# Optimization experiments

Hardware: AMD Instinct MI355X
Metric: run time of the kernel (lower is better)

## Reference

```python
import jax, jax.numpy as jnp
import numpy as np

PAIRS = [(0,1),(1,2),(2,3),(0,4),(4,5),(5,6),(0,7),(7,8),(8,9),(9,10),(8,11),(11,12),(12,13),(8,14),(14,15),(15,16)]
END_JOINTS = np.array([3, 6, 10, 13, 16])  # leaf joints gated in the trailing loop
N, DIM, HID, B = 17, 512, 384, 8192
LN_EPS = 1e-5


def _build_adj():
    A = np.zeros((N, N), np.float32)
    for p, c in PAIRS:
        A[p, c] = A[c, p] = 1.0
    A += np.eye(N, dtype=np.float32)
    dinv = 1.0 / np.sqrt(A.sum(1))
    return jnp.asarray(dinv[:, None] * A * dinv[None, :])


def setup_inputs() -> dict:
    key = jax.random.key(0)
    ks = jax.random.split(key, 8)
    return {
        "x_gcn": jax.random.normal(ks[0], (B, N, DIM), jnp.float32),
        "bone_features": jax.random.normal(ks[1], (B, N, 192), jnp.float32),
        "adj": _build_adj(),
        "g1": jnp.ones((DIM,), jnp.float32),
        "b1": jnp.zeros((DIM,), jnp.float32),
        "W1": jax.random.normal(ks[2], (2, DIM, HID), jnp.float32) * 0.02,
        "M1": jax.random.uniform(ks[3], (N, HID), jnp.float32),
        "A2_1": jnp.ones((N, N), jnp.float32),
        "bias1": jnp.zeros((HID,), jnp.float32),
        "W2": jax.random.normal(ks[4], (2, HID, DIM), jnp.float32) * 0.02,
        "M2": jax.random.uniform(ks[5], (N, DIM), jnp.float32),
        "A2_2": jnp.ones((N, N), jnp.float32),
        "bias2": jnp.zeros((DIM,), jnp.float32),
        "g2": jnp.ones((DIM,), jnp.float32),
        "b2": jnp.zeros((DIM,), jnp.float32),
    }


def _ln(x, g, b):
    m = x.mean(-1, keepdims=True)
    v = jnp.mean((x - m) ** 2, axis=-1, keepdims=True)
    return (x - m) * jax.lax.rsqrt(v + LN_EPS) * g + b


def _mgc(x, W, M, adj_base, A2, bias):
    # Modulated graph conv: separate self / neighbor transforms, per-node modulation M.
    h0 = jnp.einsum('bnc,cd->bnd', x, W[0])
    h1 = jnp.einsum('bnc,cd->bnd', x, W[1])
    adj = adj_base + A2
    adj = (adj.T + adj) * 0.5
    E = jnp.eye(N, dtype=x.dtype)
    out = jnp.einsum('vw,bwd->bvd', adj * E, M * h0) + jnp.einsum('vw,bwd->bvd', adj * (1.0 - E), M * h1)
    return out + bias


def reference(x_gcn, bone_features, adj, g1, b1, W1, M1, A2_1, bias1,
              W2, M2, A2_2, bias2, g2, b2):
    h = _ln(x_gcn, g1, b1)
    h = _mgc(h, W1, M1, adj, A2_1, bias1)
    h = jax.nn.gelu(h, approximate=False)  # torch nn.GELU default = exact erf
    h = _mgc(h, W2, M2, adj, A2_2, bias2)
    h = _ln(h, g2, b2)
    xp = x_gcn + h  # drop_path=0 -> identity

    # bone gating: first chunk(3, -1) slice, mean over channels, sigmoid gate
    c = bone_features.shape[-1]
    bone_chunk = bone_features[..., : -(-c // 3)]  # torch.chunk first piece (ceil)
    gate = jax.nn.sigmoid(bone_chunk.mean(-1, keepdims=True) * 0.01)  # (B, N, 1)
    mask = jnp.zeros((N,), xp.dtype).at[jnp.asarray(END_JOINTS)].set(1.0)
    return xp * (1.0 + 0.03 * gate * mask[None, :, None])
```

## Files before the change

### kernel.cpp

```cpp
#include <hip/hip_runtime.h>
#include <hip/hip_bf16.h>

typedef __attribute__((ext_vector_type(8))) short s16x8;
typedef __attribute__((ext_vector_type(4))) float f32x4;

typedef __attribute__((address_space(1))) void v_as1;
typedef __attribute__((address_space(3))) void v_as3;

__device__ __forceinline__ void gload16(const void* g, void* l) {
    __builtin_amdgcn_global_load_lds((const v_as1*)g, (v_as3*)l, 16, 0, 0);
}

__device__ __forceinline__ unsigned short f2bf(float f) {
    unsigned u = __float_as_uint(f);
    unsigned r = (u + 0x7FFFu + ((u >> 16) & 1u)) >> 16;
    return (unsigned short)r;
}
__device__ __forceinline__ float frombf(unsigned short u) {
    return __uint_as_float(((unsigned)u) << 16);
}

__device__ __forceinline__ float gelu_fast(float v) {
    float ax = fabsf(v) * 0.70710678118f;
    float t = __builtin_amdgcn_rcpf(fmaf(0.3275911f, ax, 1.f));
    float poly = t * fmaf(t, fmaf(t, fmaf(t, fmaf(t, 1.061405429f, -1.453152027f),
                                          1.421413741f), -0.284496736f), 0.254829592f);
    float e = exp2f(ax * ax * -1.44269504089f);
    float er = fmaf(-poly, e, 1.f);
    er = copysignf(er, v);
    return 0.5f * v * (1.f + er);
}

__global__ void prep_w1(const float* __restrict__ W1, unsigned short* __restrict__ w1t) {
    int idx = blockIdx.x * 256 + threadIdx.x;
    if (idx >= 768 * 512) return;
    int n = idx >> 9, k = idx & 511;
    int g = (n >= 384) ? 1 : 0;
    int d = n - g * 384;
    w1t[idx] = f2bf(W1[((long)g * 512 + k) * 384 + d]);
}

__global__ void prep_w2(const float* __restrict__ W2, unsigned short* __restrict__ w2t) {
    int idx = blockIdx.x * 256 + threadIdx.x;
    if (idx >= 1024 * 384) return;
    int n = idx / 384, k = idx % 384;
    int g = (n >= 512) ? 1 : 0;
    int d = n - g * 512;
    w2t[idx] = f2bf(W2[((long)g * 384 + k) * 512 + d]);
}

__global__ void prep_adj(const float* __restrict__ adj, const float* __restrict__ A2a,
                         const float* __restrict__ A2b, float* __restrict__ coef1,
                         float* __restrict__ coef2) {
    int t = threadIdx.x;
    if (t < 289) {
        int v = t / 17, w = t % 17;
        int tt = w * 17 + v;
        float s1 = 0.5f * (adj[t] + A2a[t] + adj[tt] + A2a[tt]);
        float s2 = 0.5f * (adj[t] + A2b[t] + adj[tt] + A2b[tt]);
        coef1[t] = (v == w) ? 0.f : s1;
        coef2[t] = (v == w) ? 0.f : s2;
        if (v == w) { coef1[289 + v] = s1; coef2[289 + v] = s2; }
    }
}

__global__ __launch_bounds__(256) void ln1_kernel(const float* __restrict__ x,
                                                  const float* __restrict__ g,
                                                  const float* __restrict__ b,
                                                  unsigned short* __restrict__ y, int rows) {
    int wave = threadIdx.x >> 6, lane = threadIdx.x & 63;
    long row = (long)blockIdx.x * 4 + wave;
    if (row >= rows) return;
    const float4* xr = (const float4*)(x + row * 512);
    float4 v0 = xr[lane];
    float4 v1 = xr[lane + 64];
    float s = v0.x + v0.y + v0.z + v0.w + v1.x + v1.y + v1.z + v1.w;
    float q = v0.x * v0.x + v0.y * v0.y + v0.z * v0.z + v0.w * v0.w +
              v1.x * v1.x + v1.y * v1.y + v1.z * v1.z + v1.w * v1.w;
    #pragma unroll
    for (int off = 32; off; off >>= 1) { s += __shfl_xor(s, off); q += __shfl_xor(q, off); }
    float mean = s * (1.f / 512.f);
    float var  = q * (1.f / 512.f) - mean * mean;
    float rstd = rsqrtf(var + 1e-5f);
    const float4* gr = (const float4*)g;
    const float4* br = (const float4*)b;
    ushort4* yr = (ushort4*)(y + row * 512);
    #pragma unroll
    for (int i = 0; i < 2; ++i) {
        float4 vv = i ? v1 : v0;
        float4 gg = gr[lane + 64 * i];
        float4 bb = br[lane + 64 * i];
        ushort4 o;
        o.x = f2bf((vv.x - mean) * rstd * gg.x + bb.x);
        o.y = f2bf((vv.y - mean) * rstd * gg.y + bb.y);
        o.z = f2bf((vv.z - mean) * rstd * gg.z + bb.z);
        o.w = f2bf((vv.w - mean) * rstd * gg.w + bb.w);
        yr[lane + 64 * i] = o;
    }
}

__global__ __launch_bounds__(256) void gemm_bt_kernel(const unsigned short* __restrict__ A,
                                                      const unsigned short* __restrict__ Bt,
                                                      unsigned short* __restrict__ C,
                                                      int K, int Ncols, int NBX) {
    __shared__ __align__(16) unsigned short As[128 * 64];
    __shared__ __align__(16) unsigned short Bs[128 * 64];
    const int t = threadIdx.x;
    const int lane = t & 63;
    const int w = t >> 6;
    const int wr = w >> 1, wc = w & 1;

    const int nwg = gridDim.x;
    const int q = nwg >> 3, r = nwg & 7;
    const int xcd = blockIdx.x & 7, pos = blockIdx.x >> 3;
    const int wgid = (xcd < r ? xcd * (q + 1) : r * (q + 1) + (xcd - r) * q) + pos;
    const int bx = wgid % NBX;
    const int by = wgid / NBX;
    const long row0 = (long)by * 128;
    const long col0 = (long)bx * 128;

    const int lm = lane & 15;
    const int g4 = lane >> 4;
    const int swz0 = ((g4 ^ (lm & 7)) * 8);
    const int swz1 = (((g4 + 4) ^ (lm & 7)) * 8);

    f32x4 acc[4][4];
    #pragma unroll
    for (int m = 0; m < 4; ++m)
        #pragma unroll
        for (int n = 0; n < 4; ++n) acc[m][n] = (f32x4)0.f;

    const int srow = t >> 3;
    const int sslot = (t & 7) ^ (srow & 7);
    const unsigned short* aBase = A + (row0 + srow) * K + sslot * 8;
    const unsigned short* bBase = Bt + (col0 + srow) * K + sslot * 8;
    unsigned short* aDst = &As[w * 512];
    unsigned short* bDst = &Bs[w * 512];

    const int ktiles = K >> 6;
    for (int kt = 0; kt < ktiles; ++kt) {
        const long ko = (long)kt * 64;
        __syncthreads();
        #pragma unroll
        for (int rr = 0; rr < 4; ++rr) {
            gload16(aBase + (long)(rr * 32) * K + ko, aDst + rr * 2048);
            gload16(bBase + (long)(rr * 32) * K + ko, bDst + rr * 2048);
        }
        __syncthreads();
        #pragma unroll
        for (int kk = 0; kk < 2; ++kk) {
            const int so = kk ? swz1 : swz0;
            s16x8 af[4], bfv[4];
            #pragma unroll
            for (int m = 0; m < 4; ++m)
                af[m] = *(const s16x8*)&As[(wr * 64 + m * 16 + lm) * 64 + so];
            #pragma unroll
            for (int n = 0; n < 4; ++n)
                bfv[n] = *(const s16x8*)&Bs[(wc * 64 + n * 16 + lm) * 64 + so];
            #pragma unroll
            for (int m = 0; m < 4; ++m)
                #pragma unroll
                for (int n = 0; n < 4; ++n)
                    acc[m][n] = __builtin_amdgcn_mfma_f32_16x16x32_bf16(af[m], bfv[n], acc[m][n], 0, 0, 0);
        }
    }
    const int r4 = (lane >> 4) * 4;
    #pragma unroll
    for (int m = 0; m < 4; ++m) {
        #pragma unroll
        for (int j = 0; j < 4; ++j) {
            long grow = row0 + wr * 64 + m * 16 + r4 + j;
            unsigned short* crow = C + grow * Ncols + col0 + wc * 64 + lm;
            #pragma unroll
            for (int n = 0; n < 4; ++n) crow[n * 16] = f2bf(acc[m][n][j]);
        }
    }
}

__global__ __launch_bounds__(384) void mixgelu_kernel(const unsigned short* __restrict__ h,
                                                      const float* __restrict__ M1,
                                                      const float* __restrict__ coef,
                                                      const float* __restrict__ bias,
                                                      unsigned short* __restrict__ z) {
    const int t = threadIdx.x;
    const int half = t / 192;
    const int tt = t - half * 192;
    const int d0 = tt * 2;
    const long b = blockIdx.x * 2 + half;
    const unsigned short* hb = h + b * 17 * 768;

    float ax[17], ay[17];
    const float bx = bias[d0], by = bias[d0 + 1];
    #pragma unroll
    for (int v = 0; v < 17; ++v) {
        float dg = coef[289 + v];
        float2 m = *(const float2*)(M1 + v * 384 + d0);
        ushort2 hv = *(const ushort2*)(hb + v * 768 + d0);
        ax[v] = dg * m.x * frombf(hv.x) + bx;
        ay[v] = dg * m.y * frombf(hv.y) + by;
    }
    #pragma unroll
    for (int w = 0; w < 17; ++w) {
        float2 m = *(const float2*)(M1 + w * 384 + d0);
        ushort2 hw = *(const ushort2*)(hb + w * 768 + 384 + d0);
        float px = m.x * frombf(hw.x);
        float py = m.y * frombf(hw.y);
        #pragma unroll
        for (int v = 0; v < 17; ++v) {
            float c = coef[v * 17 + w];
            ax[v] += c * px;
            ay[v] += c * py;
        }
    }
    unsigned short* zb = z + b * 17 * 384 + d0;
    #pragma unroll
    for (int v = 0; v < 17; ++v) {
        float gx = gelu_fast(ax[v]);
        float gy = gelu_fast(ay[v]);
        ushort2 o; o.x = f2bf(gx); o.y = f2bf(gy);
        *(ushort2*)(zb + v * 384) = o;
    }
}

__global__ __launch_bounds__(256) void final_kernel(const unsigned short* __restrict__ h2,
                                                    const float* __restrict__ x,
                                                    const float* __restrict__ bone,
                                                    const float* __restrict__ M2,
                                                    const float* __restrict__ coef,
                                                    const float* __restrict__ bias2,
                                                    const float* __restrict__ g2,
                                                    const float* __restrict__ b2,
                                                    float* __restrict__ out) {
    __shared__ float gate[17];
    __shared__ float red[17][8];
    const int t = threadIdx.x, lane = t & 63, wave = t >> 6;
    const int d0 = t * 2;
    const long b = blockIdx.x;

    #pragma unroll
    for (int v0 = 0; v0 < 20; v0 += 4) {
        int v = v0 + wave;
        if (v < 17) {
            float s = bone[(b * 17 + v) * 192 + lane];
            #pragma unroll
            for (int off = 32; off; off >>= 1) s += __shfl_xor(s, off);
            if (lane == 0) gate[v] = 1.f / (1.f + expf(-s * (0.01f / 64.f)));
        }
    }

    const unsigned short* hb = h2 + b * 17 * 1024;
    float ax[17], ay[17];
    const float bx = bias2[d0], by = bias2[d0 + 1];
    #pragma unroll
    for (int v = 0; v < 17; ++v) {
        float dg = coef[289 + v];
        float2 m = *(const float2*)(M2 + v * 512 + d0);
        ushort2 hv = *(const ushort2*)(hb + v * 1024 + d0);
        ax[v] = dg * m.x * frombf(hv.x) + bx;
        ay[v] = dg * m.y * frombf(hv.y) + by;
    }
    #pragma unroll
    for (int w = 0; w < 17; ++w) {
        float2 m = *(const float2*)(M2 + w * 512 + d0);
        ushort2 hw = *(const ushort2*)(hb + w * 1024 + 512 + d0);
        float px = m.x * frombf(hw.x);
        float py = m.y * frombf(hw.y);
        #pragma unroll
        for (int v = 0; v < 17; ++v) {
            float c = coef[v * 17 + w];
            ax[v] += c * px;
            ay[v] += c * py;
        }
    }
    #pragma unroll
    for (int v = 0; v < 17; ++v) {
        float s = ax[v] + ay[v];
        float q = ax[v] * ax[v] + ay[v] * ay[v];
        #pragma unroll
        for (int off = 32; off; off >>= 1) { s += __shfl_xor(s, off); q += __shfl_xor(q, off); }
        if (lane == 0) { red[v][wave] = s; red[v][4 + wave] = q; }
    }
    __syncthreads();
    const float2 gg = *(const float2*)(g2 + d0);
    const float2 bb = *(const float2*)(b2 + d0);
    const float* xb = x + b * 17 * 512 + d0;
    float* ob = out + b * 17 * 512 + d0;
    #pragma unroll
    for (int v = 0; v < 17; ++v) {
        float s = red[v][0] + red[v][1] + red[v][2] + red[v][3];
        float q = red[v][4] + red[v][5] + red[v][6] + red[v][7];
        float mean = s * (1.f / 512.f);
        float rstd = rsqrtf(q * (1.f / 512.f) - mean * mean + 1e-5f);
        const bool endj = (v == 3 || v == 6 || v == 10 || v == 13 || v == 16);
        float scale = endj ? (1.f + 0.03f * gate[v]) : 1.f;
        float2 xv = *(const float2*)(xb + v * 512);
        float ox = (xv.x + (ax[v] - mean) * rstd * gg.x + bb.x) * scale;
        float oy = (xv.y + (ay[v] - mean) * rstd * gg.y + bb.y) * scale;
        *(float2*)(ob + v * 512) = make_float2(ox, oy);
    }
}

extern "C" void kernel_launch(void* const* d_in, const int* in_sizes, int n_in,
                              void* d_out, int out_size, void* d_ws, size_t ws_size,
                              hipStream_t stream) {
    const float* x     = (const float*)d_in[0];
    const float* bone  = (const float*)d_in[1];
    const float* adj   = (const float*)d_in[2];
    const float* g1    = (const float*)d_in[3];
    const float* b1    = (const float*)d_in[4];
    const float* W1    = (const float*)d_in[5];
    const float* M1    = (const float*)d_in[6];
    const float* A21   = (const float*)d_in[7];
    const float* bias1 = (const float*)d_in[8];
    const float* W2    = (const float*)d_in[9];
    const float* M2    = (const float*)d_in[10];
    const float* A22   = (const float*)d_in[11];
    const float* bias2 = (const float*)d_in[12];
    const float* g2    = (const float*)d_in[13];
    const float* b2    = (const float*)d_in[14];
    float* out = (float*)d_out;

    char* ws = (char*)d_ws;
    size_t off = 0;
    auto alloc = [&](size_t bytes) -> char* {
        char* p = ws + off;
        off = (off + bytes + 255) & ~(size_t)255;
        return p;
    };
    unsigned short* w1t = (unsigned short*)alloc(768 * 512 * 2);
    unsigned short* w2t = (unsigned short*)alloc(1024 * 384 * 2);
    float* coef1 = (float*)alloc(306 * 4);
    float* coef2 = (float*)alloc(306 * 4);
    size_t fixed = off;

    int nc = 32;
    const int cands[6] = {1, 2, 4, 8, 16, 32};
    for (int ci = 0; ci < 6; ++ci) {
        size_t Bc = 8192 / cands[ci];
        size_t need = fixed + Bc * 17 * (512 + 768 + 384 + 1024) * 2 + 4 * 256;
        if (need <= ws_size) { nc = cands[ci]; break; }
    }
    long Bc = 8192 / nc;
    unsigned short* y  = (unsigned short*)alloc(Bc * 17 * 512 * 2);
    unsigned short* h  = (unsigned short*)alloc(Bc * 17 * 768 * 2);
    unsigned short* z  = (unsigned short*)alloc(Bc * 17 * 384 * 2);
    unsigned short* h2 = (unsigned short*)alloc(Bc * 17 * 1024 * 2);

    prep_w1<<<(768 * 512 + 255) / 256, 256, 0, stream>>>(W1, w1t);
    prep_w2<<<(1024 * 384 + 255) / 256, 256, 0, stream>>>(W2, w2t);
    prep_adj<<<1, 320, 0, stream>>>(adj, A21, A22, coef1, coef2);

    int rows = (int)(Bc * 17);
    int nby = rows / 128;
    for (int c = 0; c < nc; ++c) {
        long rb = (long)c * rows;
        ln1_kernel<<<rows / 4, 256, 0, stream>>>(x + rb * 512, g1, b1, y, rows);
        gemm_bt_kernel<<<6 * nby, 256, 0, stream>>>(y, w1t, h, 512, 768, 6);
        mixgelu_kernel<<<Bc / 2, 384, 0, stream>>>(h, M1, coef1, bias1, z);
        gemm_bt_kernel<<<8 * nby, 256, 0, stream>>>(z, w2t, h2, 384, 1024, 8);
        final_kernel<<<Bc, 256, 0, stream>>>(h2, x + rb * 512, bone + rb * 192, M2, coef2,
                                             bias2, g2, b2, out + rb * 512);
    }
}
```

Before: 693.2 us.

## Double-buffer LDS tiles in GEMM to overlap global loads with MFMA

```diff
diff --git a/kernel.cpp b/kernel.cpp
--- a/kernel.cpp
+++ b/kernel.cpp
@@ -103,8 +103,8 @@
                                                       const unsigned short* __restrict__ Bt,
                                                       unsigned short* __restrict__ C,
                                                       int K, int Ncols, int NBX) {
-    __shared__ __align__(16) unsigned short As[128 * 64];
-    __shared__ __align__(16) unsigned short Bs[128 * 64];
+    __shared__ __align__(16) unsigned short As[2][128 * 64];
+    __shared__ __align__(16) unsigned short Bs[2][128 * 64];
     const int t = threadIdx.x;
     const int lane = t & 63;
     const int w = t >> 6;
@@ -134,35 +134,51 @@
     const int sslot = (t & 7) ^ (srow & 7);
     const unsigned short* aBase = A + (row0 + srow) * K + sslot * 8;
     const unsigned short* bBase = Bt + (col0 + srow) * K + sslot * 8;
-    unsigned short* aDst = &As[w * 512];
-    unsigned short* bDst = &Bs[w * 512];
+    const int dstOff = w * 512;
 
     const int ktiles = K >> 6;
+
+    auto stage = [&](int buf, int kt) {
+        const long ko = (long)kt * 64;
+        unsigned short* aD = &As[buf][dstOff];
+        unsigned short* bD = &Bs[buf][dstOff];
+        #pragma unroll
+        for (int rr = 0; rr < 4; ++rr) {
+            gload16(aBase + (long)(rr * 32) * K + ko, aD + rr * 2048);
+            gload16(bBase + (long)(rr * 32) * K + ko, bD + rr * 2048);
+        }
+    };
+
+    stage(0, 0);
+    int p = 0;
     for (int kt = 0; kt < ktiles; ++kt) {
-        const long ko = (long)kt * 64;
-        __syncthreads();
-        #pragma unroll
-        for (int rr = 0; rr < 4; ++rr) {
-            gload16(aBase + (long)(rr * 32) * K + ko, aDst + rr * 2048);
-            gload16(bBase + (long)(rr * 32) * K + ko, bDst + rr * 2048);
-        }
-        __syncthreads();
+        __builtin_amdgcn_s_barrier();
+        if (kt + 1 < ktiles) {
+            stage(p ^ 1, kt + 1);
+            asm volatile("s_waitcnt vmcnt(8)" ::: "memory");
+        } else {
+            asm volatile("s_waitcnt vmcnt(0)" ::: "memory");
+        }
+        __builtin_amdgcn_s_barrier();
+        const unsigned short* cA = As[p];
+        const unsigned short* cB = Bs[p];
         #pragma unroll
         for (int kk = 0; kk < 2; ++kk) {
             const int so = kk ? swz1 : swz0;
             s16x8 af[4], bfv[4];
             #pragma unroll
             for (int m = 0; m < 4; ++m)
-                af[m] = *(const s16x8*)&As[(wr * 64 + m * 16 + lm) * 64 + so];
+                af[m] = *(const s16x8*)&cA[(wr * 64 + m * 16 + lm) * 64 + so];
             #pragma unroll
             for (int n = 0; n < 4; ++n)
-                bfv[n] = *(const s16x8*)&Bs[(wc * 64 + n * 16 + lm) * 64 + so];
+                bfv[n] = *(const s16x8*)&cB[(wc * 64 + n * 16 + lm) * 64 + so];
             #pragma unroll
             for (int m = 0; m < 4; ++m)
                 #pragma unroll
                 for (int n = 0; n < 4; ++n)
                     acc[m][n] = __builtin_amdgcn_mfma_f32_16x16x32_bf16(af[m], bfv[n], acc[m][n], 0, 0, 0);
         }
+        p ^= 1;
     }
     const int r4 = (lane >> 4) * 4;
     #pragma unroll
```

Result: slower. 759.1 us (+9.5%).
